# Optimization experiments

Measured on AMD Instinct MI355X. Metric: run time of the kernel, lower is better.

The kernel has to match this reference:

```python
import jax, jax.numpy as jnp
import numpy as np

ITER_STEPS = 2  # matches init_kwargs iteration_steps


def setup_inputs() -> dict:
    key = jax.random.key(0)
    ks = jax.random.split(key, 7)
    B, N, D = 16, 1024, 128
    s = 1.0 / np.sqrt(D).astype(np.float32)
    return {
        "node": jax.random.normal(ks[0], (B, N, D), jnp.float32),
        "node_mask": jax.random.randint(ks[1], (B, N), 0, 2, jnp.int32),
        "graph": jax.random.randint(ks[2], (B, N, N), 0, 2, jnp.int32),
        "w_weight": jax.random.normal(ks[3], (D, 1), jnp.float32) * s,
        "b_weight": jnp.zeros((1,), jnp.float32),
        "w_self": jax.random.normal(ks[4], (D, D), jnp.float32) * s,
        "b_self": jnp.zeros((D,), jnp.float32),
        "w_left": jax.random.normal(ks[5], (D, D), jnp.float32) * s,
        "w_right": jax.random.normal(ks[6], (D, D), jnp.float32) * s,
    }


def reference(node, node_mask, graph, w_weight, b_weight, w_self, b_self, w_left, w_right):
    B, N, D = node.shape
    dt = node.dtype
    nm = node_mask.astype(dt)
    g = graph.astype(dt)  # graph[:, :N, :N] slice is identity here
    diag = jnp.eye(N, dtype=dt)
    # pairwise validity mask, zero diagonal (no self loops)
    pair = nm[:, None, :] * nm[:, :, None] * (1.0 - diag)
    gl = pair * g            # edges present in graph
    gr = pair * (1.0 - g)    # complement edges
    nnum = gl.sum(-1) + gr.sum(-1)
    # replace_masked_values(nnum, nnum>=1, 1): avoid div-by-zero for isolated nodes
    nnum = jnp.where(nnum >= 1.0, nnum, jnp.ones((), dt))
    ws = []
    for _ in range(ITER_STEPS):
        node_weight = jax.nn.sigmoid(node @ w_weight + b_weight)[..., 0]  # [B, N]
        ws.append(node_weight)
        self_info = node @ w_self + b_self
        # replace_masked_values(weight_bcast, mask, 0) == weight * mask (mask is 0/1)
        left = jnp.einsum('bij,bjd->bid', node_weight[:, None, :] * gl, node @ w_left)
        right = jnp.einsum('bij,bjd->bid', node_weight[:, None, :] * gr, node @ w_right)
        node = jax.nn.relu(self_info + (left + right) / nnum[..., None])
    all_node_weight = jnp.stack(ws, axis=1)  # [B, ITER_STEPS, N]
    return node, all_node_weight
```

## Files before the change

kernel.cpp:

```cpp
#include <hip/hip_runtime.h>
#include <math.h>


constexpr int B = 16, N = 1024, D = 128, ITERS = 2;

typedef unsigned short u16;
typedef unsigned char u8;
typedef unsigned int u32;
typedef __attribute__((ext_vector_type(8))) short short8v;
typedef __attribute__((ext_vector_type(4))) unsigned int uint4v;
typedef __attribute__((ext_vector_type(4))) float float4v;

__device__ inline u16 f32_to_bf16(float f) {
  u32 bits = __float_as_uint(f);
  bits += 0x7FFFu + ((bits >> 16) & 1u);
  return (u16)(bits >> 16);
}

__global__ __launch_bounds__(256) void wpack_kernel(
    const float* __restrict__ w_self, const float* __restrict__ w_left,
    const float* __restrict__ w_right, const int* __restrict__ mask,
    u16* __restrict__ wsF, u16* __restrict__ wlF, u16* __restrict__ wrF,
    float* __restrict__ sb) {
  int blk = blockIdx.x, tid = threadIdx.x;
  if (blk < 12) {
    int widx = blk >> 2, seg = blk & 3;
    const float* W = (widx == 0) ? w_self : (widx == 1) ? w_left : w_right;
    u16* WF = (widx == 0) ? wsF : (widx == 1) ? wlF : wrF;
#pragma unroll
    for (int q = 0; q < 16; ++q) {
      int o = seg * 4096 + q * 256 + tid;
      int e = o & 7, lane = (o >> 3) & 63, ks = (o >> 9) & 3, cblk = o >> 11;
      int c = cblk * 16 + (lane & 15);
      int k = ks * 32 + ((lane >> 4) & 3) * 8 + e;
      WF[o] = f32_to_bf16(W[k * 128 + c]);
    }
  } else {
    int b = tid >> 4, seg = tid & 15;
    const int* mp = mask + b * N + seg * 64;
    int s = 0;
    for (int q = 0; q < 64; ++q) s += mp[q];
    float fs = (float)s;
    fs += __shfl_xor(fs, 8, 16);
    fs += __shfl_xor(fs, 4, 16);
    fs += __shfl_xor(fs, 2, 16);
    fs += __shfl_xor(fs, 1, 16);
    if (seg == 0) sb[b] = fs;
  }
}

__device__ __forceinline__ void prep_body(
    float (*nlds)[132], float* wmrow, float* invrow, int b, int rt, int tid,
    const int* __restrict__ mask, const float* __restrict__ w_weight,
    const float* __restrict__ b_weight, const float* __restrict__ b_self,
    const u16* __restrict__ wsF, const u16* __restrict__ wlF,
    const u16* __restrict__ wrF, const float* __restrict__ sb,
    float* __restrict__ outw_t, float* __restrict__ nsadj, u16* __restrict__ xF,
    float* __restrict__ part) {
  int r0 = rt * 16;
  if (tid < 128) {
    int r = tid >> 3, jj = tid & 7;
    float acc = 0.f;
#pragma unroll
    for (int q = 0; q < 4; ++q) {
      float4 wv = *(const float4*)(w_weight + jj * 16 + q * 4);
      const float* np = &nlds[r][jj * 16 + q * 4];
      acc += np[0] * wv.x + np[1] * wv.y + np[2] * wv.z + np[3] * wv.w;
    }
    acc += __shfl_xor(acc, 4, 8);
    acc += __shfl_xor(acc, 2, 8);
    acc += __shfl_xor(acc, 1, 8);
    if (jj == 0) {
      float w = 1.f / (1.f + expf(-(acc + b_weight[0])));
      outw_t[b * (ITERS * N) + r0 + r] = w;
      float nm = (float)mask[b * N + r0 + r];
      float nnum = fmaxf(nm * (sb[b] - nm), 1.f);
      wmrow[r] = w * nm;
      invrow[r] = nm / nnum;
    }
  }
  __syncthreads();

  int w = tid >> 6, lane = tid & 63;
  int l15 = lane & 15, lg = lane >> 4;
  int ch = w * 32;

  short8v af[4];
#pragma unroll
  for (int ks = 0; ks < 4; ++ks) {
    float tmp[8];
    *(float4*)&tmp[0] = *(const float4*)&nlds[l15][ks * 32 + lg * 8];
    *(float4*)&tmp[4] = *(const float4*)&nlds[l15][ks * 32 + lg * 8 + 4];
    short8v t;
#pragma unroll
    for (int e = 0; e < 8; ++e) t[e] = (short)f32_to_bf16(tmp[e]);
    af[ks] = t;
  }

  float4v aNR[2], aNL[2], aNS[2];
#define RUN_GEMM(WF, ACC)                                                          \
  {                                                                                \
    _Pragma("unroll") for (int cf = 0; cf < 2; ++cf) {                             \
      ACC[cf] = (float4v){0.f, 0.f, 0.f, 0.f};                                     \
      int cblk = w * 2 + cf;                                                       \
      const u16* bp = (WF) + (((cblk * 4) * 64 + lane) << 3);                      \
      _Pragma("unroll") for (int ks = 0; ks < 4; ++ks) {                           \
        short8v bf = *(const short8v*)(bp + ks * 512);                             \
        ACC[cf] =                                                                  \
            __builtin_amdgcn_mfma_f32_16x16x32_bf16(af[ks], bf, ACC[cf], 0, 0, 0); \
      }                                                                            \
    }                                                                              \
  }
  RUN_GEMM(wrF, aNR);
  RUN_GEMM(wlF, aNL);
  RUN_GEMM(wsF, aNS);
#undef RUN_GEMM

  float wmv[4], invv[4];
#pragma unroll
  for (int j = 0; j < 4; ++j) {
    int rloc = lg * 4 + j;
    wmv[j] = wmrow[rloc];
    invv[j] = invrow[rloc];
  }
  int kch = rt >> 1;
  int lane_f = ((rt & 1) * 2 + (lg >> 1)) * 16;
  int e0 = (lg & 1) * 4;
  float pv[2] = {0.f, 0.f};
#pragma unroll
  for (int cf = 0; cf < 2; ++cf) {
    int col = ch + cf * 16 + l15;
    float bsv = b_self[col];
    u16 xb[4];
#pragma unroll
    for (int j = 0; j < 4; ++j) {
      float x = wmv[j] * (aNL[cf][j] - aNR[cf][j]);
      float v = wmv[j] * aNR[cf][j];
      pv[cf] += v;
      nsadj[((size_t)b * N + r0 + lg * 4 + j) * D + col] =
          aNS[cf][j] + bsv - invv[j] * v;
      xb[j] = f32_to_bf16(x);
    }
    int cblk = w * 2 + cf;
    size_t fi = ((((size_t)b * 8 + cblk) * 32 + kch) * 64 + lane_f + l15) * 8 + e0;
    *(ushort4*)&xF[fi] = *(ushort4*)&xb[0];
  }
#pragma unroll
  for (int cf = 0; cf < 2; ++cf) {
    pv[cf] += __shfl_xor(pv[cf], 16);
    pv[cf] += __shfl_xor(pv[cf], 32);
  }
  if (lg == 0) {
#pragma unroll
    for (int cf = 0; cf < 2; ++cf)
      part[((size_t)b * 64 + rt) * 128 + ch + cf * 16 + l15] = pv[cf];
  }
}

__device__ __forceinline__ void agg_tile(
    const u8* __restrict__ gpk, const u16* __restrict__ xF,
    const float* __restrict__ part, const float* __restrict__ sb,
    const int* __restrict__ mask, const float* __restrict__ nsadj, int b, int r0,
    int tid, float (*accbuf)[16][132], float* vt_s, float ov[8]) {
  if (tid < 128) {
    float s = 0.f;
#pragma unroll
    for (int p = 0; p < 64; ++p) s += part[((size_t)b * 64 + p) * 128 + tid];
    vt_s[tid] = s;
  }
  int w = tid >> 6, lane = tid & 63;
  int l15 = lane & 15, lg = lane >> 4;
  int ks = w;
  const u8* gr = gpk + ((size_t)b * N + r0 + l15) * 128 + lg * 32 + ks * 8;
  uint2 q = *(const uint2*)gr;
  u32 qa[2] = {q.x, q.y};

  const u16* bp[8];
#pragma unroll
  for (int cf = 0; cf < 8; ++cf)
    bp[cf] = xF + ((((size_t)b * 8 + cf) * 32 + ks * 8) * 64 + lane) * 8;

  float4v acc[8] = {{0.f, 0.f, 0.f, 0.f}, {0.f, 0.f, 0.f, 0.f},
                    {0.f, 0.f, 0.f, 0.f}, {0.f, 0.f, 0.f, 0.f},
                    {0.f, 0.f, 0.f, 0.f}, {0.f, 0.f, 0.f, 0.f},
                    {0.f, 0.f, 0.f, 0.f}, {0.f, 0.f, 0.f, 0.f}};
#pragma unroll
  for (int cl = 0; cl < 8; ++cl) {
    u32 by = (qa[cl >> 2] >> ((cl & 3) * 8)) & 255u;
    u32 e0 = ((by & 1u) ? 0x3F80u : 0u) | ((by & 2u) ? 0x3F800000u : 0u);
    u32 e1 = ((by & 4u) ? 0x3F80u : 0u) | ((by & 8u) ? 0x3F800000u : 0u);
    u32 e2 = ((by & 16u) ? 0x3F80u : 0u) | ((by & 32u) ? 0x3F800000u : 0u);
    u32 e3 = ((by & 64u) ? 0x3F80u : 0u) | ((by & 128u) ? 0x3F800000u : 0u);
    uint4v ev = {e0, e1, e2, e3};
    short8v a = __builtin_bit_cast(short8v, ev);
    int koff = cl * 512;
#pragma unroll
    for (int cf = 0; cf < 8; ++cf) {
      short8v bf = *(const short8v*)(bp[cf] + koff);
      acc[cf] = __builtin_amdgcn_mfma_f32_16x16x32_bf16(a, bf, acc[cf], 0, 0, 0);
    }
  }
#pragma unroll
  for (int cf = 0; cf < 8; ++cf)
#pragma unroll
    for (int j = 0; j < 4; ++j) accbuf[w][lg * 4 + j][cf * 16 + l15] = acc[cf][j];
  __syncthreads();

  int row = w * 4 + (lane >> 4);
  int colb = (tid & 15) * 8;
  int orow = r0 + row;
  float nm = (float)mask[b * N + orow];
  float sbv = sb[b];
  float nnum = fmaxf(nm * (sbv - nm), 1.f);
  float inv = nm / nnum;
  const float* nsp = nsadj + ((size_t)b * N + orow) * D + colb;
  float4 n0 = *(const float4*)nsp;
  float4 n1 = *(const float4*)(nsp + 4);
  float nsa[8] = {n0.x, n0.y, n0.z, n0.w, n1.x, n1.y, n1.z, n1.w};
#pragma unroll
  for (int e = 0; e < 8; ++e) {
    int c = colb + e;
    float m = accbuf[0][row][c] + accbuf[1][row][c] + accbuf[2][row][c] +
              accbuf[3][row][c] + vt_s[c];
    ov[e] = fmaxf(nsa[e] + inv * m, 0.f);
  }
}

__global__ __launch_bounds__(256, 4) void prep_pack_kernel(
    const float* __restrict__ node, const int* __restrict__ graph,
    const int* __restrict__ mask, const float* __restrict__ w_weight,
    const float* __restrict__ b_weight, const float* __restrict__ b_self,
    const u16* __restrict__ wsF, const u16* __restrict__ wlF,
    const u16* __restrict__ wrF, const float* __restrict__ sb,
    u8* __restrict__ gpk, float* __restrict__ outw, float* __restrict__ nsadjA,
    u16* __restrict__ xFA, float* __restrict__ partA) {
  __shared__ float nlds[16][132];
  __shared__ float wmrow[16], invrow[16];
  __shared__ u32 lbw[2][32];
  int tid = threadIdx.x;
  int b = blockIdx.x >> 6;
  int rt = blockIdx.x & 63;
  int r0 = rt * 16;

  {
    int rl = tid >> 7, j = tid & 127;
#pragma unroll
    for (int pp = 0; pp < 8; ++pp) {
      int i = r0 + pp * 2 + rl;
      const int* gp = graph + ((size_t)b * N + i) * N + j * 8;
      int4 a = *(const int4*)gp;
      int4 c = *(const int4*)(gp + 4);
      u32 by = (u32)(a.x != 0) | ((u32)(a.y != 0) << 1) | ((u32)(a.z != 0) << 2) |
               ((u32)(a.w != 0) << 3) | ((u32)(c.x != 0) << 4) |
               ((u32)(c.y != 0) << 5) | ((u32)(c.z != 0) << 6) |
               ((u32)(c.w != 0) << 7);
      if (j == (i >> 3)) by &= ~(1u << (i & 7));
      ((u8*)&lbw[rl][0])[(j & 3) * 32 + (j >> 2)] = (u8)by;
      __syncthreads();
      if (tid < 64) {
        int rl2 = tid >> 5, d = tid & 31;
        ((u32*)gpk)[((size_t)b * N + r0 + pp * 2 + rl2) * 32 + d] = lbw[rl2][d];
      }
      __syncthreads();
    }
  }

  const float* nbase = node + ((size_t)b * N + r0) * D;
#pragma unroll
  for (int p = 0; p < 2; ++p) {
    int g = p * 256 + tid;
    int row = g >> 5, c4 = g & 31;
    *(float4*)&nlds[row][c4 * 4] = *(const float4*)(nbase + row * 128 + c4 * 4);
  }
  __syncthreads();

  prep_body(nlds, wmrow, invrow, b, rt, tid, mask, w_weight, b_weight, b_self, wsF,
            wlF, wrF, sb, outw, nsadjA, xFA, partA);
}

__global__ __launch_bounds__(256, 3) void agg_prep_kernel(
    const u8* __restrict__ gpk, const int* __restrict__ mask,
    const float* __restrict__ w_weight, const float* __restrict__ b_weight,
    const float* __restrict__ b_self, const u16* __restrict__ wsF,
    const u16* __restrict__ wlF, const u16* __restrict__ wrF,
    const float* __restrict__ sb, const float* __restrict__ nsadjA,
    const u16* __restrict__ xFA, const float* __restrict__ partA,
    float* __restrict__ outw, float* __restrict__ nsadjB, u16* __restrict__ xFB,
    float* __restrict__ partB) {
  __shared__ float accbuf[4][16][132];
  __shared__ float vt_s[128];
  __shared__ float nlds[16][132];
  __shared__ float wmrow[16], invrow[16];
  int tid = threadIdx.x;
  int b = blockIdx.x >> 6;
  int rt = blockIdx.x & 63;
  int r0 = rt * 16;

  float ov[8];
  agg_tile(gpk, xFA, partA, sb, mask, nsadjA, b, r0, tid, accbuf, vt_s, ov);

  int row = (tid >> 6) * 4 + ((tid & 63) >> 4);
  int colb = (tid & 15) * 8;
#pragma unroll
  for (int e = 0; e < 8; ++e) nlds[row][colb + e] = ov[e];
  __syncthreads();

  prep_body(nlds, wmrow, invrow, b, rt, tid, mask, w_weight, b_weight, b_self, wsF,
            wlF, wrF, sb, outw + N , nsadjB, xFB, partB);
}

__global__ __launch_bounds__(256, 4) void agg_fin_kernel(
    const u8* __restrict__ gpk, const int* __restrict__ mask,
    const float* __restrict__ sb, const float* __restrict__ nsadjB,
    const u16* __restrict__ xFB, const float* __restrict__ partB,
    float* __restrict__ out) {
  __shared__ float accbuf[4][16][132];
  __shared__ float vt_s[128];
  int tid = threadIdx.x;
  int b = blockIdx.x >> 6;
  int rt = blockIdx.x & 63;
  int r0 = rt * 16;

  float ov[8];
  agg_tile(gpk, xFB, partB, sb, mask, nsadjB, b, r0, tid, accbuf, vt_s, ov);

  int row = (tid >> 6) * 4 + ((tid & 63) >> 4);
  int colb = (tid & 15) * 8;
  float* op = out + ((size_t)b * N + r0 + row) * D + colb;
  float4 o0 = {ov[0], ov[1], ov[2], ov[3]};
  float4 o1 = {ov[4], ov[5], ov[6], ov[7]};
  *(float4*)op = o0;
  *(float4*)(op + 4) = o1;
}

extern "C" void kernel_launch(void* const* d_in, const int* in_sizes, int n_in,
                              void* d_out, int out_size, void* d_ws, size_t ws_size,
                              hipStream_t stream) {
  const float* node0 = (const float*)d_in[0];
  const int* mask = (const int*)d_in[1];
  const int* graph = (const int*)d_in[2];
  const float* w_weight = (const float*)d_in[3];
  const float* b_weight = (const float*)d_in[4];
  const float* w_self = (const float*)d_in[5];
  const float* b_self = (const float*)d_in[6];
  const float* w_left = (const float*)d_in[7];
  const float* w_right = (const float*)d_in[8];
  float* out = (float*)d_out;
  float* outw = out + (size_t)B * N * D;

  char* ws = (char*)d_ws;
  const size_t MB = 1024 * 1024;
  float* nsadjA = (float*)ws;
  float* nsadjB = (float*)(ws + 8 * MB);
  u16* xFA = (u16*)(ws + 16 * MB);
  u16* xFB = (u16*)(ws + 20 * MB);
  u8* gpk = (u8*)(ws + 24 * MB);
  u16* wsF = (u16*)(ws + 26 * MB);
  u16* wlF = wsF + 16384;
  u16* wrF = wlF + 16384;
  float* partA = (float*)(ws + 26 * MB + 3 * 32768);
  float* partB = partA + (size_t)B * 64 * 128;
  float* sb = partB + (size_t)B * 64 * 128;

  wpack_kernel<<<13, 256, 0, stream>>>(w_self, w_left, w_right, mask, wsF, wlF,
                                       wrF, sb);
  prep_pack_kernel<<<1024, 256, 0, stream>>>(node0, graph, mask, w_weight,
                                             b_weight, b_self, wsF, wlF, wrF, sb,
                                             gpk, outw, nsadjA, xFA, partA);
  agg_prep_kernel<<<1024, 256, 0, stream>>>(gpk, mask, w_weight, b_weight, b_self,
                                            wsF, wlF, wrF, sb, nsadjA, xFA, partA,
                                            outw, nsadjB, xFB, partB);
  agg_fin_kernel<<<1024, 256, 0, stream>>>(gpk, mask, sb, nsadjB, xFB, partB, out);
}
```

Measured before the change: 71.28 us.

## Aggregate 32-row tiles per block and batch graph bit-packing stores

The aggregation kernels now give each block 32 rows instead of 16. Each wave covers one 16-row fragment over half of K, so the K-split partial reduction drops from four waves to two, and the blocks reuse the xF B-fragments across two row fragments. agg_prep then runs prep_body twice per block, once per 16-row half. In prep_pack, the node tile is loaded into registers before graph packing and all 16 packed rows are staged in LDS with a single barrier, replacing two barriers per row pair. The grid is halved to 512 blocks with launch bounds of 2, which lowers parallelism and occupancy and adds register pressure.

```diff
diff --git a/kernel.cpp b/kernel.cpp
--- a/kernel.cpp
+++ b/kernel.cpp
@@ -157,75 +157,6 @@
   }
 }
 
-__device__ __forceinline__ void agg_tile(
-    const u8* __restrict__ gpk, const u16* __restrict__ xF,
-    const float* __restrict__ part, const float* __restrict__ sb,
-    const int* __restrict__ mask, const float* __restrict__ nsadj, int b, int r0,
-    int tid, float (*accbuf)[16][132], float* vt_s, float ov[8]) {
-  if (tid < 128) {
-    float s = 0.f;
-#pragma unroll
-    for (int p = 0; p < 64; ++p) s += part[((size_t)b * 64 + p) * 128 + tid];
-    vt_s[tid] = s;
-  }
-  int w = tid >> 6, lane = tid & 63;
-  int l15 = lane & 15, lg = lane >> 4;
-  int ks = w;
-  const u8* gr = gpk + ((size_t)b * N + r0 + l15) * 128 + lg * 32 + ks * 8;
-  uint2 q = *(const uint2*)gr;
-  u32 qa[2] = {q.x, q.y};
-
-  const u16* bp[8];
-#pragma unroll
-  for (int cf = 0; cf < 8; ++cf)
-    bp[cf] = xF + ((((size_t)b * 8 + cf) * 32 + ks * 8) * 64 + lane) * 8;
-
-  float4v acc[8] = {{0.f, 0.f, 0.f, 0.f}, {0.f, 0.f, 0.f, 0.f},
-                    {0.f, 0.f, 0.f, 0.f}, {0.f, 0.f, 0.f, 0.f},
-                    {0.f, 0.f, 0.f, 0.f}, {0.f, 0.f, 0.f, 0.f},
-                    {0.f, 0.f, 0.f, 0.f}, {0.f, 0.f, 0.f, 0.f}};
-#pragma unroll
-  for (int cl = 0; cl < 8; ++cl) {
-    u32 by = (qa[cl >> 2] >> ((cl & 3) * 8)) & 255u;
-    u32 e0 = ((by & 1u) ? 0x3F80u : 0u) | ((by & 2u) ? 0x3F800000u : 0u);
-    u32 e1 = ((by & 4u) ? 0x3F80u : 0u) | ((by & 8u) ? 0x3F800000u : 0u);
-    u32 e2 = ((by & 16u) ? 0x3F80u : 0u) | ((by & 32u) ? 0x3F800000u : 0u);
-    u32 e3 = ((by & 64u) ? 0x3F80u : 0u) | ((by & 128u) ? 0x3F800000u : 0u);
-    uint4v ev = {e0, e1, e2, e3};
-    short8v a = __builtin_bit_cast(short8v, ev);
-    int koff = cl * 512;
-#pragma unroll
-    for (int cf = 0; cf < 8; ++cf) {
-      short8v bf = *(const short8v*)(bp[cf] + koff);
-      acc[cf] = __builtin_amdgcn_mfma_f32_16x16x32_bf16(a, bf, acc[cf], 0, 0, 0);
-    }
-  }
-#pragma unroll
-  for (int cf = 0; cf < 8; ++cf)
-#pragma unroll
-    for (int j = 0; j < 4; ++j) accbuf[w][lg * 4 + j][cf * 16 + l15] = acc[cf][j];
-  __syncthreads();
-
-  int row = w * 4 + (lane >> 4);
-  int colb = (tid & 15) * 8;
-  int orow = r0 + row;
-  float nm = (float)mask[b * N + orow];
-  float sbv = sb[b];
-  float nnum = fmaxf(nm * (sbv - nm), 1.f);
-  float inv = nm / nnum;
-  const float* nsp = nsadj + ((size_t)b * N + orow) * D + colb;
-  float4 n0 = *(const float4*)nsp;
-  float4 n1 = *(const float4*)(nsp + 4);
-  float nsa[8] = {n0.x, n0.y, n0.z, n0.w, n1.x, n1.y, n1.z, n1.w};
-#pragma unroll
-  for (int e = 0; e < 8; ++e) {
-    int c = colb + e;
-    float m = accbuf[0][row][c] + accbuf[1][row][c] + accbuf[2][row][c] +
-              accbuf[3][row][c] + vt_s[c];
-    ov[e] = fmaxf(nsa[e] + inv * m, 0.f);
-  }
-}
-
 __global__ __launch_bounds__(256, 4) void prep_pack_kernel(
     const float* __restrict__ node, const int* __restrict__ graph,
     const int* __restrict__ mask, const float* __restrict__ w_weight,
@@ -236,11 +167,19 @@
     u16* __restrict__ xFA, float* __restrict__ partA) {
   __shared__ float nlds[16][132];
   __shared__ float wmrow[16], invrow[16];
-  __shared__ u32 lbw[2][32];
+  __shared__ u32 lbw[16][32];
   int tid = threadIdx.x;
   int b = blockIdx.x >> 6;
   int rt = blockIdx.x & 63;
   int r0 = rt * 16;
+
+  float4 nreg[2];
+  const float* nbase = node + ((size_t)b * N + r0) * D;
+#pragma unroll
+  for (int p = 0; p < 2; ++p) {
+    int g = p * 256 + tid;
+    nreg[p] = *(const float4*)(nbase + (g >> 5) * 128 + (g & 31) * 4);
+  }
 
   {
     int rl = tid >> 7, j = tid & 127;
@@ -255,22 +194,19 @@
                ((u32)(c.y != 0) << 5) | ((u32)(c.z != 0) << 6) |
                ((u32)(c.w != 0) << 7);
       if (j == (i >> 3)) by &= ~(1u << (i & 7));
-      ((u8*)&lbw[rl][0])[(j & 3) * 32 + (j >> 2)] = (u8)by;
-      __syncthreads();
-      if (tid < 64) {
-        int rl2 = tid >> 5, d = tid & 31;
-        ((u32*)gpk)[((size_t)b * N + r0 + pp * 2 + rl2) * 32 + d] = lbw[rl2][d];
-      }
-      __syncthreads();
-    }
-  }
-
-  const float* nbase = node + ((size_t)b * N + r0) * D;
+      ((u8*)&lbw[pp * 2 + rl][0])[(j & 3) * 32 + (j >> 2)] = (u8)by;
+    }
+  }
+  __syncthreads();
+  {
+    int row = tid >> 4, d = (tid & 15) * 2;
+    uint2 wv = {lbw[row][d], lbw[row][d + 1]};
+    *(uint2*)&((u32*)gpk)[((size_t)b * N + r0 + row) * 32 + d] = wv;
+  }
 #pragma unroll
   for (int p = 0; p < 2; ++p) {
     int g = p * 256 + tid;
-    int row = g >> 5, c4 = g & 31;
-    *(float4*)&nlds[row][c4 * 4] = *(const float4*)(nbase + row * 128 + c4 * 4);
+    *(float4*)&nlds[g >> 5][(g & 31) * 4] = nreg[p];
   }
   __syncthreads();
 
@@ -278,7 +214,47 @@
             wlF, wrF, sb, outw, nsadjA, xFA, partA);
 }
 
-__global__ __launch_bounds__(256, 3) void agg_prep_kernel(
+#define AGG32_CORE(GPK, XF, PART)                                                  \
+  if (tid < 128) {                                          \
+    float s = 0.f;                                                                 \
+    _Pragma("unroll") for (int p = 0; p < 64; ++p) s +=                            \
+        (PART)[((size_t)b * 64 + p) * 128 + tid];                                  \
+    vt_s[tid] = s;                                                                 \
+  }                                                                                \
+  int w = tid >> 6, lane = tid & 63;                                               \
+  int l15 = lane & 15, lg = lane >> 4;                                             \
+  int rf = w & 1, kh = w >> 1;                                                     \
+  const u8* gr =                                                                   \
+      (GPK) + ((size_t)b * N + r0 + rf * 16 + l15) * 128 + lg * 32 + kh * 16;      \
+  uint4 qv = *(const uint4*)gr;                                                    \
+  u32 qa[4] = {qv.x, qv.y, qv.z, qv.w};                                            \
+  const u16* bp[8];                                                                \
+  _Pragma("unroll") for (int cf = 0; cf < 8; ++cf) bp[cf] =                        \
+      (XF) + ((((size_t)b * 8 + cf) * 32 + kh * 16) * 64 + lane) * 8;              \
+  float4v acc[8] = {{0.f, 0.f, 0.f, 0.f}, {0.f, 0.f, 0.f, 0.f},                    \
+                    {0.f, 0.f, 0.f, 0.f}, {0.f, 0.f, 0.f, 0.f},                    \
+                    {0.f, 0.f, 0.f, 0.f}, {0.f, 0.f, 0.f, 0.f},                    \
+                    {0.f, 0.f, 0.f, 0.f}, {0.f, 0.f, 0.f, 0.f}};                   \
+  _Pragma("unroll") for (int cl = 0; cl < 16; ++cl) {                              \
+    u32 by = (qa[cl >> 2] >> ((cl & 3) * 8)) & 255u;                               \
+    u32 e0 = ((by & 1u) ? 0x3F80u : 0u) | ((by & 2u) ? 0x3F800000u : 0u);          \
+    u32 e1 = ((by & 4u) ? 0x3F80u : 0u) | ((by & 8u) ? 0x3F800000u : 0u);          \
+    u32 e2 = ((by & 16u) ? 0x3F80u : 0u) | ((by & 32u) ? 0x3F800000u : 0u);        \
+    u32 e3 = ((by & 64u) ? 0x3F80u : 0u) | ((by & 128u) ? 0x3F800000u : 0u);       \
+    uint4v ev = {e0, e1, e2, e3};                                                  \
+    short8v a = __builtin_bit_cast(short8v, ev);                                   \
+    int koff = cl * 512;                                                           \
+    _Pragma("unroll") for (int cf = 0; cf < 8; ++cf) {                             \
+      short8v bf = *(const short8v*)(bp[cf] + koff);                               \
+      acc[cf] = __builtin_amdgcn_mfma_f32_16x16x32_bf16(a, bf, acc[cf], 0, 0, 0);  \
+    }                                                                              \
+  }                                                                                \
+  _Pragma("unroll") for (int cf = 0; cf < 8; ++cf)                                 \
+      _Pragma("unroll") for (int j = 0; j < 4; ++j)                                \
+          accbuf[w][lg * 4 + j][cf * 16 + l15] = acc[cf][j];                       \
+  __syncthreads();
+
+__global__ __launch_bounds__(256, 2) void agg_prep_kernel(
     const u8* __restrict__ gpk, const int* __restrict__ mask,
     const float* __restrict__ w_weight, const float* __restrict__ b_weight,
     const float* __restrict__ b_self, const u16* __restrict__ wsF,
@@ -289,27 +265,47 @@
     float* __restrict__ partB) {
   __shared__ float accbuf[4][16][132];
   __shared__ float vt_s[128];
-  __shared__ float nlds[16][132];
+  __shared__ float nlds[32][132];
   __shared__ float wmrow[16], invrow[16];
   int tid = threadIdx.x;
-  int b = blockIdx.x >> 6;
-  int rt = blockIdx.x & 63;
-  int r0 = rt * 16;
-
-  float ov[8];
-  agg_tile(gpk, xFA, partA, sb, mask, nsadjA, b, r0, tid, accbuf, vt_s, ov);
-
-  int row = (tid >> 6) * 4 + ((tid & 63) >> 4);
-  int colb = (tid & 15) * 8;
-#pragma unroll
-  for (int e = 0; e < 8; ++e) nlds[row][colb + e] = ov[e];
-  __syncthreads();
-
-  prep_body(nlds, wmrow, invrow, b, rt, tid, mask, w_weight, b_weight, b_self, wsF,
-            wlF, wrF, sb, outw + N , nsadjB, xFB, partB);
-}
-
-__global__ __launch_bounds__(256, 4) void agg_fin_kernel(
+  int b = blockIdx.x >> 5;
+  int rt32 = blockIdx.x & 31;
+  int r0 = rt32 * 32;
+
+  AGG32_CORE(gpk, xFA, partA)
+
+  {
+    int row = tid >> 3, colq = (tid & 7) * 16;
+    int rfe = row >> 4, r15 = row & 15;
+    int orow = r0 + row;
+    float nm = (float)mask[b * N + orow];
+    float sbv = sb[b];
+    float nnum = fmaxf(nm * (sbv - nm), 1.f);
+    float inv = nm / nnum;
+    const float* nsp = nsadjA + ((size_t)b * N + orow) * D + colq;
+#pragma unroll
+    for (int q = 0; q < 4; ++q) {
+      float4 ns = *(const float4*)(nsp + q * 4);
+      float nsa[4] = {ns.x, ns.y, ns.z, ns.w};
+#pragma unroll
+      for (int e = 0; e < 4; ++e) {
+        int c = colq + q * 4 + e;
+        float m = accbuf[rfe][r15][c] + accbuf[2 + rfe][r15][c] + vt_s[c];
+        nlds[row][c] = fmaxf(nsa[e] + inv * m, 0.f);
+      }
+    }
+  }
+  __syncthreads();
+
+  prep_body(nlds, wmrow, invrow, b, rt32 * 2, tid, mask, w_weight, b_weight,
+            b_self, wsF, wlF, wrF, sb, outw + N, nsadjB, xFB, partB);
+  __syncthreads();
+  prep_body((float(*)[132]) & nlds[16][0], wmrow, invrow, b, rt32 * 2 + 1, tid,
+            mask, w_weight, b_weight, b_self, wsF, wlF, wrF, sb, outw + N, nsadjB,
+            xFB, partB);
+}
+
+__global__ __launch_bounds__(256, 2) void agg_fin_kernel(
     const u8* __restrict__ gpk, const int* __restrict__ mask,
     const float* __restrict__ sb, const float* __restrict__ nsadjB,
     const u16* __restrict__ xFB, const float* __restrict__ partB,
@@ -317,20 +313,38 @@
   __shared__ float accbuf[4][16][132];
   __shared__ float vt_s[128];
   int tid = threadIdx.x;
-  int b = blockIdx.x >> 6;
-  int rt = blockIdx.x & 63;
-  int r0 = rt * 16;
-
-  float ov[8];
-  agg_tile(gpk, xFB, partB, sb, mask, nsadjB, b, r0, tid, accbuf, vt_s, ov);
-
-  int row = (tid >> 6) * 4 + ((tid & 63) >> 4);
-  int colb = (tid & 15) * 8;
-  float* op = out + ((size_t)b * N + r0 + row) * D + colb;
-  float4 o0 = {ov[0], ov[1], ov[2], ov[3]};
-  float4 o1 = {ov[4], ov[5], ov[6], ov[7]};
-  *(float4*)op = o0;
-  *(float4*)(op + 4) = o1;
+  int b = blockIdx.x >> 5;
+  int rt32 = blockIdx.x & 31;
+  int r0 = rt32 * 32;
+
+  AGG32_CORE(gpk, xFB, partB)
+
+  {
+    int row = tid >> 3, colq = (tid & 7) * 16;
+    int rfe = row >> 4, r15 = row & 15;
+    int orow = r0 + row;
+    float nm = (float)mask[b * N + orow];
+    float sbv = sb[b];
+    float nnum = fmaxf(nm * (sbv - nm), 1.f);
+    float inv = nm / nnum;
+    const float* nsp = nsadjB + ((size_t)b * N + orow) * D + colq;
+    float* op = out + ((size_t)b * N + orow) * D + colq;
+#pragma unroll
+    for (int q = 0; q < 4; ++q) {
+      float4 ns = *(const float4*)(nsp + q * 4);
+      float nsa[4] = {ns.x, ns.y, ns.z, ns.w};
+      float4 o;
+      float oa[4];
+#pragma unroll
+      for (int e = 0; e < 4; ++e) {
+        int c = colq + q * 4 + e;
+        float m = accbuf[rfe][r15][c] + accbuf[2 + rfe][r15][c] + vt_s[c];
+        oa[e] = fmaxf(nsa[e] + inv * m, 0.f);
+      }
+      o.x = oa[0]; o.y = oa[1]; o.z = oa[2]; o.w = oa[3];
+      *(float4*)(op + q * 4) = o;
+    }
+  }
 }
 
 extern "C" void kernel_launch(void* const* d_in, const int* in_sizes, int n_in,
@@ -367,8 +381,8 @@
   prep_pack_kernel<<<1024, 256, 0, stream>>>(node0, graph, mask, w_weight,
                                              b_weight, b_self, wsF, wlF, wrF, sb,
                                              gpk, outw, nsadjA, xFA, partA);
-  agg_prep_kernel<<<1024, 256, 0, stream>>>(gpk, mask, w_weight, b_weight, b_self,
-                                            wsF, wlF, wrF, sb, nsadjA, xFA, partA,
-                                            outw, nsadjB, xFB, partB);
-  agg_fin_kernel<<<1024, 256, 0, stream>>>(gpk, mask, sb, nsadjB, xFB, partB, out);
-}
+  agg_prep_kernel<<<512, 256, 0, stream>>>(gpk, mask, w_weight, b_weight, b_self,
+                                           wsF, wlF, wrF, sb, nsadjA, xFA, partA,
+                                           outw, nsadjB, xFB, partB);
+  agg_fin_kernel<<<512, 256, 0, stream>>>(gpk, mask, sb, nsadjB, xFB, partB, out);
+}
```

Result: slower. 99.85 us (+40.1%).

## Software-prefetch xF B-fragments in aggregation loop and remap blocks across batches

Applied to the files above, without the earlier changes.

The aggregation MFMA loop now loads the next k-step's eight B fragments into registers while the current step's MFMAs run, using double-buffered register arrays. This hides global load latency behind matrix math. Block-to-(batch, row-tile) mapping is also changed so consecutive block IDs interleave eight batches, which is meant to spread work across XCDs/L2 slices. It costs extra VGPRs, which may lower occupancy under the launch bounds of 3-4 waves.

```diff
diff --git a/kernel.cpp b/kernel.cpp
--- a/kernel.cpp
+++ b/kernel.cpp
@@ -15,6 +15,12 @@
   u32 bits = __float_as_uint(f);
   bits += 0x7FFFu + ((bits >> 16) & 1u);
   return (u16)(bits >> 16);
+}
+
+__device__ __forceinline__ void map_brt(int blk, int& b, int& rt) {
+  int slot = blk >> 3;
+  b = ((slot >> 6) << 3) | (blk & 7);
+  rt = slot & 63;
 }
 
 __global__ __launch_bounds__(256) void wpack_kernel(
@@ -175,17 +181,23 @@
   uint2 q = *(const uint2*)gr;
   u32 qa[2] = {q.x, q.y};
 
-  const u16* bp[8];
-#pragma unroll
-  for (int cf = 0; cf < 8; ++cf)
-    bp[cf] = xF + ((((size_t)b * 8 + cf) * 32 + ks * 8) * 64 + lane) * 8;
+  const u16* xb = xF + ((((size_t)b * 8) * 32 + ks * 8) * 64 + lane) * 8;
 
   float4v acc[8] = {{0.f, 0.f, 0.f, 0.f}, {0.f, 0.f, 0.f, 0.f},
                     {0.f, 0.f, 0.f, 0.f}, {0.f, 0.f, 0.f, 0.f},
                     {0.f, 0.f, 0.f, 0.f}, {0.f, 0.f, 0.f, 0.f},
                     {0.f, 0.f, 0.f, 0.f}, {0.f, 0.f, 0.f, 0.f}};
+  short8v bcur[8], bnxt[8];
+#pragma unroll
+  for (int cf = 0; cf < 8; ++cf)
+    bcur[cf] = *(const short8v*)(xb + cf * 16384);
 #pragma unroll
   for (int cl = 0; cl < 8; ++cl) {
+    if (cl + 1 < 8) {
+#pragma unroll
+      for (int cf = 0; cf < 8; ++cf)
+        bnxt[cf] = *(const short8v*)(xb + cf * 16384 + (cl + 1) * 512);
+    }
     u32 by = (qa[cl >> 2] >> ((cl & 3) * 8)) & 255u;
     u32 e0 = ((by & 1u) ? 0x3F80u : 0u) | ((by & 2u) ? 0x3F800000u : 0u);
     u32 e1 = ((by & 4u) ? 0x3F80u : 0u) | ((by & 8u) ? 0x3F800000u : 0u);
@@ -193,12 +205,11 @@
     u32 e3 = ((by & 64u) ? 0x3F80u : 0u) | ((by & 128u) ? 0x3F800000u : 0u);
     uint4v ev = {e0, e1, e2, e3};
     short8v a = __builtin_bit_cast(short8v, ev);
-    int koff = cl * 512;
-#pragma unroll
-    for (int cf = 0; cf < 8; ++cf) {
-      short8v bf = *(const short8v*)(bp[cf] + koff);
-      acc[cf] = __builtin_amdgcn_mfma_f32_16x16x32_bf16(a, bf, acc[cf], 0, 0, 0);
-    }
+#pragma unroll
+    for (int cf = 0; cf < 8; ++cf)
+      acc[cf] = __builtin_amdgcn_mfma_f32_16x16x32_bf16(a, bcur[cf], acc[cf], 0, 0, 0);
+#pragma unroll
+    for (int cf = 0; cf < 8; ++cf) bcur[cf] = bnxt[cf];
   }
 #pragma unroll
   for (int cf = 0; cf < 8; ++cf)
@@ -238,8 +249,8 @@
   __shared__ float wmrow[16], invrow[16];
   __shared__ u32 lbw[2][32];
   int tid = threadIdx.x;
-  int b = blockIdx.x >> 6;
-  int rt = blockIdx.x & 63;
+  int b, rt;
+  map_brt(blockIdx.x, b, rt);
   int r0 = rt * 16;
 
   {
@@ -292,8 +303,8 @@
   __shared__ float nlds[16][132];
   __shared__ float wmrow[16], invrow[16];
   int tid = threadIdx.x;
-  int b = blockIdx.x >> 6;
-  int rt = blockIdx.x & 63;
+  int b, rt;
+  map_brt(blockIdx.x, b, rt);
   int r0 = rt * 16;
 
   float ov[8];
@@ -317,8 +328,8 @@
   __shared__ float accbuf[4][16][132];
   __shared__ float vt_s[128];
   int tid = threadIdx.x;
-  int b = blockIdx.x >> 6;
-  int rt = blockIdx.x & 63;
+  int b, rt;
+  map_brt(blockIdx.x, b, rt);
   int r0 = rt * 16;
 
   float ov[8];
```

Measured after the change: 66.05 us. 1.08x faster.
